# Optimization experiments

Hardware: AMD Instinct MI355X
Metric: run time of the kernel (lower is better)

## Reference

```python
import jax, jax.numpy as jnp
import numpy as np

EPS_MSG = 1e-7   # GENConv message eps
EPS_SM = 1e-16   # scatter_softmax denom eps
EPS_BN = 1e-5    # BatchNorm1d eps


def genconv(x, src, dst, t, W1, W2, gamma, beta):
    """One GENConv (aggr='softmax', learn_t, edge_attr=None, bias=False)."""
    n = x.shape[0]
    # message: relu(x_j) + eps over edges  [E, d]
    msg = jax.nn.relu(x[src]) + EPS_MSG
    # softmax over edges sharing a destination, per feature, temperature t
    logits = msg * t
    m = jax.ops.segment_max(logits, dst, num_segments=n)
    m = jnp.where(jnp.isfinite(m), m, 0.0)          # empty segments -> 0
    w = jnp.exp(logits - m[dst])
    denom = jax.ops.segment_sum(w, dst, num_segments=n) + EPS_SM
    aggr = jax.ops.segment_sum(w * msg, dst, num_segments=n) / denom
    # update: MLP(aggr + x); MLP = Lin(d,2d) -> BN -> ReLU -> Lin(2d,d)
    h = aggr + x
    h1 = h @ W1
    mean = jnp.mean(h1, axis=0)
    var = jnp.var(h1, axis=0)
    h1 = (h1 - mean) * jax.lax.rsqrt(var + EPS_BN) * gamma + beta
    h1 = jax.nn.relu(h1)
    return h1 @ W2


def setup_inputs() -> dict:
    key = jax.random.key(0)
    ks = jax.random.split(key, 4)
    N, E, D = 100000, 800000, 128
    x = jax.random.normal(ks[0], (N, D), dtype=jnp.float32)
    edge_index = jax.random.randint(ks[1], (2, E), 0, N, dtype=jnp.int64)
    t_all = jnp.ones((4,), dtype=jnp.float32)  # learn_t init 1.0
    W1_all = jax.random.normal(ks[2], (4, D, 2 * D), dtype=jnp.float32) * (1.0 / np.sqrt(D))
    W2_all = jax.random.normal(ks[3], (4, 2 * D, D), dtype=jnp.float32) * (1.0 / np.sqrt(2 * D))
    gamma_all = jnp.ones((4, 2 * D), dtype=jnp.float32)
    beta_all = jnp.zeros((4, 2 * D), dtype=jnp.float32)
    return {"x": x, "edge_index": edge_index, "t_all": t_all,
            "W1_all": W1_all, "W2_all": W2_all,
            "gamma_all": gamma_all, "beta_all": beta_all}


def reference(x, edge_index, t_all, W1_all, W2_all, gamma_all, beta_all):
    src, dst = edge_index[0], edge_index[1]
    n_aggr = 2
    h = x
    for i in range(n_aggr):
        h = genconv(h, src, dst, t_all[i], W1_all[i], W2_all[i], gamma_all[i], beta_all[i])
        h = jax.nn.relu(h)
        # dropout: identity (inference)
    mu = genconv(h, src, dst, t_all[2], W1_all[2], W2_all[2], gamma_all[2], beta_all[2])
    logstd = genconv(h, src, dst, t_all[3], W1_all[3], W2_all[3], gamma_all[3], beta_all[3])
    return (mu, logstd)
```

## Files before the change

### kernel.cpp

```cpp
#include <hip/hip_runtime.h>
#include <math.h>

#define D 128
#define H 256
#define NSLOT 64

typedef short s16x8 __attribute__((ext_vector_type(8)));
typedef float f32x4 __attribute__((ext_vector_type(4)));
typedef unsigned int u32x2 __attribute__((ext_vector_type(2)));
typedef unsigned short u16;
typedef unsigned int u32;

__device__ __forceinline__ u16 f2b(float f) {
    union { float f; unsigned u; } c;
    c.f = f;
    unsigned u = c.u + 0x7FFFu + ((c.u >> 16) & 1u);
    return (u16)(u >> 16);
}
__device__ __forceinline__ float b2f(u16 h) {
    union { unsigned u; float f; } c;
    c.u = ((unsigned)h) << 16;
    return c.f;
}
__device__ __forceinline__ float blo(u32 p) {
    union { unsigned u; float f; } c;
    c.u = p << 16;
    return c.f;
}
__device__ __forceinline__ float bhi(u32 p) {
    union { unsigned u; float f; } c;
    c.u = p & 0xFFFF0000u;
    return c.f;
}


__global__ __launch_bounds__(256) void k_count(const int* __restrict__ dstA,
                                               int* __restrict__ deg, int E) {
    int e = blockIdx.x * 256 + threadIdx.x;
    if (e < E) atomicAdd(&deg[dstA[e]], 1);
}

__global__ __launch_bounds__(1024) void k_scan1(const int* __restrict__ deg,
                                                int* __restrict__ rowptr,
                                                int* __restrict__ bsum, int N) {
    __shared__ int tmp[1024];
    int t = threadIdx.x;
    int i = blockIdx.x * 1024 + t;
    int v = (i < N) ? deg[i] : 0;
    tmp[t] = v;
    __syncthreads();
    #pragma unroll
    for (int off = 1; off < 1024; off <<= 1) {
        int u = (t >= off) ? tmp[t - off] : 0;
        __syncthreads();
        tmp[t] += u;
        __syncthreads();
    }
    if (i < N) rowptr[i] = tmp[t] - v;
    if (t == 1023) bsum[blockIdx.x] = tmp[1023];
}

__global__ __launch_bounds__(1024) void k_scan2(int* __restrict__ bsum, int B) {
    __shared__ int sums[1024];
    int t = threadIdx.x;
    int chunk = (B + 1023) >> 10;
    int beg = t * chunk;
    int end = beg + chunk;
    if (end > B) end = B;
    int s = 0;
    for (int i = beg; i < end; ++i) s += bsum[i];
    sums[t] = s;
    __syncthreads();
    #pragma unroll
    for (int off = 1; off < 1024; off <<= 1) {
        int v = (t >= off) ? sums[t - off] : 0;
        __syncthreads();
        sums[t] += v;
        __syncthreads();
    }
    int run = (t == 0) ? 0 : sums[t - 1];
    for (int i = beg; i < end; ++i) {
        int v = bsum[i];
        bsum[i] = run;
        run += v;
    }
}

__global__ __launch_bounds__(1024) void k_scan3(int* __restrict__ rowptr,
                                                const int* __restrict__ bsum,
                                                int* __restrict__ deg,
                                                int N, int E) {
    int i = blockIdx.x * 1024 + threadIdx.x;
    if (i < N) {
        rowptr[i] += bsum[blockIdx.x];
        deg[i] = 0;
    } else if (i == N) {
        rowptr[N] = E;
    }
}

__global__ __launch_bounds__(256) void k_scatter(const int* __restrict__ srcA,
                                                 const int* __restrict__ dstA,
                                                 const int* __restrict__ rowptr,
                                                 int* __restrict__ cnt,
                                                 int* __restrict__ srcs, int E) {
    int e = blockIdx.x * 256 + threadIdx.x;
    if (e < E) {
        int d = dstA[e];
        int p = rowptr[d] + atomicAdd(&cnt[d], 1);
        srcs[p] = srcA[e];
    }
}


__global__ __launch_bounds__(256) void k_cvtprep(const float* __restrict__ x,
                                                 u16* __restrict__ xb,
                                                 const float* __restrict__ W1_all,
                                                 const float* __restrict__ W2_all,
                                                 u16* __restrict__ WT1,
                                                 u16* __restrict__ WT2,
                                                 int* __restrict__ deg,
                                                 int n4, int N) {
    int id = blockIdx.x * 256 + threadIdx.x;
    if (id < N) deg[id] = 0;
    if (id < n4) {
        float4 v = ((const float4*)x)[id];
        xb[id * 4 + 0] = f2b(v.x);
        xb[id * 4 + 1] = f2b(v.y);
        xb[id * 4 + 2] = f2b(v.z);
        xb[id * 4 + 3] = f2b(v.w);
    } else {
        int p = id - n4;
        if (p < 131072) {
            int l = p >> 15, rem = p & 32767, n = rem >> 7, k = rem & 127;
            WT1[p] = f2b(W1_all[l * 32768 + k * 256 + n]);
        } else if (p < 262144) {
            int p2 = p - 131072;
            int l = p2 >> 15, rem = p2 & 32767, n = rem >> 8, k = rem & 255;
            WT2[p2] = f2b(W2_all[l * 32768 + k * 128 + n]);
        }
    }
}


__global__ __launch_bounds__(256) void k_edge(const u16* __restrict__ hin,
                                              const int* __restrict__ rowptr,
                                              const int* __restrict__ srcs,
                                              const float* __restrict__ tptr,
                                              u16* __restrict__ g,
                                              float* __restrict__ psum,
                                              float* __restrict__ pss, int N) {
    if (blockIdx.x < NSLOT) {
        psum[blockIdx.x * 256 + threadIdx.x] = 0.f;
        pss[blockIdx.x * 256 + threadIdx.x] = 0.f;
    }
    int u = blockIdx.x * 4 + (threadIdx.x >> 6);
    if (u >= N) return;
    u = __builtin_amdgcn_readfirstlane(u);
    int lane = threadIdx.x & 63;
    const u32* hin32 = (const u32*)hin;
    float t = *tptr;
    int beg = rowptr[u], end = rowptr[u + 1];
    int cnt = end - beg;

    u32 pu = hin32[(size_t)u * 64 + lane];

    float s0 = 0.f, s1 = 0.f, sn0 = 0.f, sn1 = 0.f;

    for (int b = 0; b < cnt; b += 64) {
        int nb = cnt - b;
        if (nb > 64) nb = 64;
        int sv = (b + lane < cnt) ? srcs[beg + b + lane] : 0;
        for (int ib = 0; ib < nb; ib += 16) {
            int m = nb - ib;
            if (m > 16) m = 16;
            u32 pr[16];
            #pragma unroll
            for (int j = 0; j < 16; ++j) {
                if (j < m) {
                    int vi = __builtin_amdgcn_readlane(sv, ib + j);
                    pr[j] = hin32[(size_t)vi * 64 + lane];
                }
            }
            #pragma unroll
            for (int j = 0; j < 16; ++j) {
                if (j < m) {
                    u32 p = pr[j];
                    float v0 = fmaxf(blo(p), 0.f) + 1e-7f;
                    float v1 = fmaxf(bhi(p), 0.f) + 1e-7f;
                    float w0 = __expf(v0 * t), w1 = __expf(v1 * t);
                    s0 += w0; s1 += w1;
                    sn0 = fmaf(w0, v0, sn0);
                    sn1 = fmaf(w1, v1, sn1);
                }
            }
        }
    }

    bool has = (cnt > 0);
    bool good = (s0 >= 1e-8f) && (s0 <= 1e26f) && (s1 >= 1e-8f) && (s1 <= 1e26f)
                && (sn0 - sn0 == 0.0f) && (sn1 - sn1 == 0.0f);
    if (__any(has && !good)) {
        float m0 = -3.0e38f, m1 = -3.0e38f;
        s0 = s1 = sn0 = sn1 = 0.f;
        for (int e = beg; e < end; ++e) {
            int v = srcs[e];
            u32 p = hin32[(size_t)v * 64 + lane];
            float v0 = fmaxf(blo(p), 0.f) + 1e-7f;
            float v1 = fmaxf(bhi(p), 0.f) + 1e-7f;
            float l0 = v0 * t, l1 = v1 * t;
            float nm0 = fmaxf(m0, l0), nm1 = fmaxf(m1, l1);
            float a0 = __expf(m0 - nm0), a1 = __expf(m1 - nm1);
            float w0 = __expf(l0 - nm0), w1 = __expf(l1 - nm1);
            s0 = s0 * a0 + w0;           s1 = s1 * a1 + w1;
            sn0 = sn0 * a0 + w0 * v0;    sn1 = sn1 * a1 + w1 * v1;
            m0 = nm0; m1 = nm1;
        }
    }

    float aggr0 = sn0 / (s0 + 1e-16f);
    float aggr1 = sn1 / (s1 + 1e-16f);
    float o0 = aggr0 + blo(pu);
    float o1 = aggr1 + bhi(pu);
    ((u32*)g)[(size_t)u * 64 + lane] = (u32)f2b(o0) | ((u32)f2b(o1) << 16);
}


__global__ __launch_bounds__(256) void k_mm1(const u16* __restrict__ A,
                                             const u16* __restrict__ WT,
                                             u16* __restrict__ C,
                                             float* __restrict__ psum,
                                             float* __restrict__ pss, int M) {
    __shared__ u16 As[128][72];
    __shared__ u16 Bs[128][72];
    __shared__ float csumA[128], cssA[128], csumB[128], cssB[128];
    int row0 = blockIdx.x * 128, n0 = blockIdx.y * 128;
    int tid = threadIdx.x;
    int lane = tid & 63, w = tid >> 6;
    int r0w = (w & 1) * 64, c0w = (w >> 1) * 64;
    int q = lane >> 4, ml = lane & 15;

    f32x4 acc[4][4];
    #pragma unroll
    for (int i = 0; i < 4; ++i)
        #pragma unroll
        for (int j = 0; j < 4; ++j) acc[i][j] = f32x4{0.f, 0.f, 0.f, 0.f};

    for (int kk = 0; kk < 128; kk += 64) {
        #pragma unroll
        for (int i = 0; i < 4; ++i) {
            int r = i * 32 + (tid >> 3);
            int c8 = (tid & 7) * 8;
            s16x8 va = s16x8{0, 0, 0, 0, 0, 0, 0, 0};
            if (row0 + r < M)
                va = *reinterpret_cast<const s16x8*>(&A[(size_t)(row0 + r) * 128 + kk + c8]);
            *reinterpret_cast<s16x8*>(&As[r][c8]) = va;
            s16x8 vb = *reinterpret_cast<const s16x8*>(&WT[(size_t)(n0 + r) * 128 + kk + c8]);
            *reinterpret_cast<s16x8*>(&Bs[r][c8]) = vb;
        }
        __syncthreads();
        #pragma unroll
        for (int ks = 0; ks < 64; ks += 32) {
            s16x8 af[4], bfr[4];
            #pragma unroll
            for (int rt = 0; rt < 4; ++rt)
                af[rt] = *reinterpret_cast<const s16x8*>(&As[r0w + rt * 16 + ml][ks + q * 8]);
            #pragma unroll
            for (int ct = 0; ct < 4; ++ct)
                bfr[ct] = *reinterpret_cast<const s16x8*>(&Bs[c0w + ct * 16 + ml][ks + q * 8]);
            #pragma unroll
            for (int rt = 0; rt < 4; ++rt)
                #pragma unroll
                for (int ct = 0; ct < 4; ++ct)
                    acc[rt][ct] = __builtin_amdgcn_mfma_f32_16x16x32_bf16(
                        bfr[ct], af[rt], acc[rt][ct], 0, 0, 0);
        }
        __syncthreads();
    }

    #pragma unroll
    for (int rt = 0; rt < 4; ++rt) {
        int row = row0 + r0w + rt * 16 + ml;
        if (row < M) {
            #pragma unroll
            for (int ct = 0; ct < 4; ++ct) {
                f32x4 a = acc[rt][ct];
                u32x2 p;
                p.x = (u32)f2b(a[0]) | ((u32)f2b(a[1]) << 16);
                p.y = (u32)f2b(a[2]) | ((u32)f2b(a[3]) << 16);
                int col = n0 + c0w + ct * 16 + q * 4;
                *reinterpret_cast<u32x2*>(&C[(size_t)row * H + col]) = p;
            }
        }
    }

    float sp[16], ssp[16];
    #pragma unroll
    for (int ct = 0; ct < 4; ++ct)
        #pragma unroll
        for (int r = 0; r < 4; ++r) {
            float s = 0.f, ss = 0.f;
            #pragma unroll
            for (int rt = 0; rt < 4; ++rt) {
                float v = acc[rt][ct][r];
                s += v;
                ss += v * v;
            }
            sp[ct * 4 + r] = s;
            ssp[ct * 4 + r] = ss;
        }
    #pragma unroll
    for (int msk = 1; msk < 16; msk <<= 1) {
        #pragma unroll
        for (int i = 0; i < 16; ++i) {
            sp[i] += __shfl_xor(sp[i], msk);
            ssp[i] += __shfl_xor(ssp[i], msk);
        }
    }
    if (ml == 0) {
        float* cs = (w & 1) ? csumB : csumA;
        float* cq = (w & 1) ? cssB : cssA;
        #pragma unroll
        for (int ct = 0; ct < 4; ++ct)
            #pragma unroll
            for (int r = 0; r < 4; ++r) {
                int col = c0w + ct * 16 + q * 4 + r;
                cs[col] = sp[ct * 4 + r];
                cq[col] = ssp[ct * 4 + r];
            }
    }
    __syncthreads();
    if (tid < 128) {
        int slot = blockIdx.x & (NSLOT - 1);
        atomicAdd(&psum[(size_t)slot * 256 + n0 + tid], csumA[tid] + csumB[tid]);
        atomicAdd(&pss[(size_t)slot * 256 + n0 + tid], cssA[tid] + cssB[tid]);
    }
}


__global__ __launch_bounds__(256) void k_mm2(const u16* __restrict__ H1,
                                             const float* __restrict__ psum,
                                             const float* __restrict__ pss,
                                             const float* __restrict__ gamma,
                                             const float* __restrict__ beta,
                                             const u16* __restrict__ WT,
                                             float* __restrict__ outf,
                                             u16* __restrict__ outb, int M) {
    __shared__ u16 As[128][72];
    __shared__ u16 Bs[128][72];
    __shared__ float sc_s[H], sh_s[H];
    int row0 = blockIdx.x * 128;
    int tid = threadIdx.x;
    int lane = tid & 63, w = tid >> 6;
    int r0w = (w & 1) * 64, c0w = (w >> 1) * 64;
    int q = lane >> 4, ml = lane & 15;

    {
        float s = 0.f, ss = 0.f;
        #pragma unroll 8
        for (int b = 0; b < NSLOT; ++b) {
            s += psum[b * 256 + tid];
            ss += pss[b * 256 + tid];
        }
        float inv = 1.0f / (float)M;
        float mean = s * inv;
        float var = ss * inv - mean * mean;
        if (var < 0.f) var = 0.f;
        float rstd = rsqrtf(var + 1e-5f);
        float sc = rstd * gamma[tid];
        sc_s[tid] = sc;
        sh_s[tid] = beta[tid] - mean * sc;
    }
    __syncthreads();

    f32x4 acc[4][4];
    #pragma unroll
    for (int i = 0; i < 4; ++i)
        #pragma unroll
        for (int j = 0; j < 4; ++j) acc[i][j] = f32x4{0.f, 0.f, 0.f, 0.f};

    for (int kk = 0; kk < 256; kk += 64) {
        #pragma unroll
        for (int i = 0; i < 4; ++i) {
            int r = i * 32 + (tid >> 3);
            int c8 = (tid & 7) * 8;
            s16x8 o = s16x8{0, 0, 0, 0, 0, 0, 0, 0};
            if (row0 + r < M) {
                s16x8 v = *reinterpret_cast<const s16x8*>(&H1[(size_t)(row0 + r) * H + kk + c8]);
                #pragma unroll
                for (int j = 0; j < 8; ++j) {
                    float f = b2f((u16)v[j]) * sc_s[kk + c8 + j] + sh_s[kk + c8 + j];
                    o[j] = (short)f2b(fmaxf(f, 0.f));
                }
            }
            *reinterpret_cast<s16x8*>(&As[r][c8]) = o;
            s16x8 vb = *reinterpret_cast<const s16x8*>(&WT[(size_t)r * H + kk + c8]);
            *reinterpret_cast<s16x8*>(&Bs[r][c8]) = vb;
        }
        __syncthreads();
        #pragma unroll
        for (int ks = 0; ks < 64; ks += 32) {
            s16x8 af[4], bfr[4];
            #pragma unroll
            for (int rt = 0; rt < 4; ++rt)
                af[rt] = *reinterpret_cast<const s16x8*>(&As[r0w + rt * 16 + ml][ks + q * 8]);
            #pragma unroll
            for (int ct = 0; ct < 4; ++ct)
                bfr[ct] = *reinterpret_cast<const s16x8*>(&Bs[c0w + ct * 16 + ml][ks + q * 8]);
            #pragma unroll
            for (int rt = 0; rt < 4; ++rt)
                #pragma unroll
                for (int ct = 0; ct < 4; ++ct)
                    acc[rt][ct] = __builtin_amdgcn_mfma_f32_16x16x32_bf16(
                        bfr[ct], af[rt], acc[rt][ct], 0, 0, 0);
        }
        __syncthreads();
    }

    #pragma unroll
    for (int rt = 0; rt < 4; ++rt) {
        int row = row0 + r0w + rt * 16 + ml;
        if (row < M) {
            #pragma unroll
            for (int ct = 0; ct < 4; ++ct) {
                f32x4 a = acc[rt][ct];
                int col = c0w + ct * 16 + q * 4;
                if (outb) {
                    u32x2 p;
                    p.x = (u32)f2b(fmaxf(a[0], 0.f)) | ((u32)f2b(fmaxf(a[1], 0.f)) << 16);
                    p.y = (u32)f2b(fmaxf(a[2], 0.f)) | ((u32)f2b(fmaxf(a[3], 0.f)) << 16);
                    *reinterpret_cast<u32x2*>(&outb[(size_t)row * D + col]) = p;
                } else {
                    *reinterpret_cast<f32x4*>(&outf[(size_t)row * D + col]) = a;
                }
            }
        }
    }
}


extern "C" void kernel_launch(void* const* d_in, const int* in_sizes, int n_in,
                              void* d_out, int out_size, void* d_ws, size_t ws_size,
                              hipStream_t stream) {
    const float* x         = (const float*)d_in[0];
    const int*   ei        = (const int*)d_in[1];
    const float* t_all     = (const float*)d_in[2];
    const float* W1_all    = (const float*)d_in[3];
    const float* W2_all    = (const float*)d_in[4];
    const float* gamma_all = (const float*)d_in[5];
    const float* beta_all  = (const float*)d_in[6];

    int N = in_sizes[0] / D;
    int E = in_sizes[1] / 2;
    float* out = (float*)d_out;

    char* ws = (char*)d_ws;
    size_t off = 0;
    auto alloc = [&](size_t bytes) -> void* {
        void* p = ws + off;
        off += (bytes + 255) & ~(size_t)255;
        return p;
    };
    int B = (N + 1023) >> 10;
    int* rowptr = (int*)alloc((size_t)(N + 1) * 4);
    int* deg    = (int*)alloc((size_t)N * 4);
    int* srcs   = (int*)alloc((size_t)E * 4);
    int* bsum   = (int*)alloc((size_t)(B + 1) * 4);
    u16* xb     = (u16*)alloc((size_t)N * D * 2);
    u16* a0     = (u16*)alloc((size_t)N * D * 2);
    u16* a1     = (u16*)alloc((size_t)N * D * 2);
    u16* g      = (u16*)alloc((size_t)N * D * 2);
    u16* h1     = (u16*)alloc((size_t)N * H * 2);
    u16* WT1    = (u16*)alloc((size_t)4 * H * D * 2);
    u16* WT2    = (u16*)alloc((size_t)4 * D * H * 2);
    float* psum = (float*)alloc((size_t)NSLOT * 256 * 4);
    float* pss  = (float*)alloc((size_t)NSLOT * 256 * 4);
    (void)ws_size; (void)n_in; (void)out_size;

    const int* srcA = ei;
    const int* dstA = ei + E;

    int n4 = N * D / 4;
    k_cvtprep<<<(n4 + 262144 + 255) / 256, 256, 0, stream>>>(
        x, xb, W1_all, W2_all, WT1, WT2, deg, n4, N);

    k_count<<<(E + 255) / 256, 256, 0, stream>>>(dstA, deg, E);
    k_scan1<<<B, 1024, 0, stream>>>(deg, rowptr, bsum, N);
    k_scan2<<<1, 1024, 0, stream>>>(bsum, B);
    k_scan3<<<(N + 1 + 1023) / 1024, 1024, 0, stream>>>(rowptr, bsum, deg, N, E);
    k_scatter<<<(E + 255) / 256, 256, 0, stream>>>(srcA, dstA, rowptr, deg, srcs, E);

    float* out0 = out;
    float* out1 = out + (size_t)N * D;

    int gx = (N + 127) / 128;
    for (int layer = 0; layer < 4; ++layer) {
        const u16* hin = (layer == 0) ? xb : (layer == 1 ? a0 : a1);
        k_edge<<<(N + 3) / 4, 256, 0, stream>>>(hin, rowptr, srcs, t_all + layer,
                                                g, psum, pss, N);

        k_mm1<<<dim3(gx, 2), 256, 0, stream>>>(g, WT1 + (size_t)layer * H * D, h1,
                                               psum, pss, N);

        float* outf = nullptr;
        u16*   outb = nullptr;
        if (layer == 0)      outb = a0;
        else if (layer == 1) outb = a1;
        else if (layer == 2) outf = out0;
        else                 outf = out1;

        k_mm2<<<dim3(gx, 1), 256, 0, stream>>>(h1, psum, pss,
                                               gamma_all + (size_t)layer * H,
                                               beta_all + (size_t)layer * H,
                                               WT2 + (size_t)layer * D * H,
                                               outf, outb, N);
    }
}
```

Before: 797.6 us.

## Load MFMA operands directly from global memory, dropping LDS staging in GEMMs

Both GEMM kernels (mm1 and mm2) no longer stage A and W tiles in shared memory with __syncthreads. Each lane now loads its MFMA fragments straight from global memory, with a bounds-checked path for the tail block in mm1 and clamped row pointers in mm2. This removes the LDS round trip and the barriers and should raise occupancy. In exchange, each wave loads data that other waves in the block also load, so the kernels rely more on L1/L2 bandwidth, and mm2 repeats its BN affine transform per wave.

```diff
diff --git a/kernel.cpp b/kernel.cpp
--- a/kernel.cpp
+++ b/kernel.cpp
@@ -231,8 +231,6 @@
                                              u16* __restrict__ C,
                                              float* __restrict__ psum,
                                              float* __restrict__ pss, int M) {
-    __shared__ u16 As[128][72];
-    __shared__ u16 Bs[128][72];
     __shared__ float csumA[128], cssA[128], csumB[128], cssB[128];
     int row0 = blockIdx.x * 128, n0 = blockIdx.y * 128;
     int tid = threadIdx.x;
@@ -246,28 +244,19 @@
         #pragma unroll
         for (int j = 0; j < 4; ++j) acc[i][j] = f32x4{0.f, 0.f, 0.f, 0.f};
 
-    for (int kk = 0; kk < 128; kk += 64) {
-        #pragma unroll
-        for (int i = 0; i < 4; ++i) {
-            int r = i * 32 + (tid >> 3);
-            int c8 = (tid & 7) * 8;
-            s16x8 va = s16x8{0, 0, 0, 0, 0, 0, 0, 0};
-            if (row0 + r < M)
-                va = *reinterpret_cast<const s16x8*>(&A[(size_t)(row0 + r) * 128 + kk + c8]);
-            *reinterpret_cast<s16x8*>(&As[r][c8]) = va;
-            s16x8 vb = *reinterpret_cast<const s16x8*>(&WT[(size_t)(n0 + r) * 128 + kk + c8]);
-            *reinterpret_cast<s16x8*>(&Bs[r][c8]) = vb;
-        }
-        __syncthreads();
-        #pragma unroll
-        for (int ks = 0; ks < 64; ks += 32) {
+    const u16* Ab = A + (size_t)(row0 + r0w + ml) * D + q * 8;
+    const u16* Bb = WT + (size_t)(n0 + c0w + ml) * D + q * 8;
+
+    if (row0 + 128 <= M) {
+        #pragma unroll 2
+        for (int ks = 0; ks < 128; ks += 32) {
             s16x8 af[4], bfr[4];
             #pragma unroll
             for (int rt = 0; rt < 4; ++rt)
-                af[rt] = *reinterpret_cast<const s16x8*>(&As[r0w + rt * 16 + ml][ks + q * 8]);
+                af[rt] = *reinterpret_cast<const s16x8*>(&Ab[(size_t)rt * 16 * D + ks]);
             #pragma unroll
             for (int ct = 0; ct < 4; ++ct)
-                bfr[ct] = *reinterpret_cast<const s16x8*>(&Bs[c0w + ct * 16 + ml][ks + q * 8]);
+                bfr[ct] = *reinterpret_cast<const s16x8*>(&Bb[(size_t)ct * 16 * D + ks]);
             #pragma unroll
             for (int rt = 0; rt < 4; ++rt)
                 #pragma unroll
@@ -275,7 +264,27 @@
                     acc[rt][ct] = __builtin_amdgcn_mfma_f32_16x16x32_bf16(
                         bfr[ct], af[rt], acc[rt][ct], 0, 0, 0);
         }
-        __syncthreads();
+    } else {
+        #pragma unroll 2
+        for (int ks = 0; ks < 128; ks += 32) {
+            s16x8 af[4], bfr[4];
+            #pragma unroll
+            for (int rt = 0; rt < 4; ++rt) {
+                int row = row0 + r0w + rt * 16 + ml;
+                af[rt] = (row < M)
+                    ? *reinterpret_cast<const s16x8*>(&Ab[(size_t)rt * 16 * D + ks])
+                    : s16x8{0, 0, 0, 0, 0, 0, 0, 0};
+            }
+            #pragma unroll
+            for (int ct = 0; ct < 4; ++ct)
+                bfr[ct] = *reinterpret_cast<const s16x8*>(&Bb[(size_t)ct * 16 * D + ks]);
+            #pragma unroll
+            for (int rt = 0; rt < 4; ++rt)
+                #pragma unroll
+                for (int ct = 0; ct < 4; ++ct)
+                    acc[rt][ct] = __builtin_amdgcn_mfma_f32_16x16x32_bf16(
+                        bfr[ct], af[rt], acc[rt][ct], 0, 0, 0);
+        }
     }
 
     #pragma unroll
@@ -346,8 +355,6 @@
                                              const u16* __restrict__ WT,
                                              float* __restrict__ outf,
                                              u16* __restrict__ outb, int M) {
-    __shared__ u16 As[128][72];
-    __shared__ u16 Bs[128][72];
     __shared__ float sc_s[H], sh_s[H];
     int row0 = blockIdx.x * 128;
     int tid = threadIdx.x;
@@ -379,42 +386,39 @@
         #pragma unroll
         for (int j = 0; j < 4; ++j) acc[i][j] = f32x4{0.f, 0.f, 0.f, 0.f};
 
-    for (int kk = 0; kk < 256; kk += 64) {
-        #pragma unroll
-        for (int i = 0; i < 4; ++i) {
-            int r = i * 32 + (tid >> 3);
-            int c8 = (tid & 7) * 8;
-            s16x8 o = s16x8{0, 0, 0, 0, 0, 0, 0, 0};
-            if (row0 + r < M) {
-                s16x8 v = *reinterpret_cast<const s16x8*>(&H1[(size_t)(row0 + r) * H + kk + c8]);
-                #pragma unroll
-                for (int j = 0; j < 8; ++j) {
-                    float f = b2f((u16)v[j]) * sc_s[kk + c8 + j] + sh_s[kk + c8 + j];
-                    o[j] = (short)f2b(fmaxf(f, 0.f));
-                }
-            }
-            *reinterpret_cast<s16x8*>(&As[r][c8]) = o;
-            s16x8 vb = *reinterpret_cast<const s16x8*>(&WT[(size_t)r * H + kk + c8]);
-            *reinterpret_cast<s16x8*>(&Bs[r][c8]) = vb;
-        }
-        __syncthreads();
-        #pragma unroll
-        for (int ks = 0; ks < 64; ks += 32) {
-            s16x8 af[4], bfr[4];
-            #pragma unroll
-            for (int rt = 0; rt < 4; ++rt)
-                af[rt] = *reinterpret_cast<const s16x8*>(&As[r0w + rt * 16 + ml][ks + q * 8]);
+    const u16* Ab[4];
+    #pragma unroll
+    for (int rt = 0; rt < 4; ++rt) {
+        int row = row0 + r0w + rt * 16 + ml;
+        if (row >= M) row = M - 1;
+        Ab[rt] = H1 + (size_t)row * H + q * 8;
+    }
+    const u16* Bb = WT + (size_t)(c0w + ml) * H + q * 8;
+
+    #pragma unroll 2
+    for (int ks = 0; ks < 256; ks += 32) {
+        s16x8 af[4], bfr[4];
+        #pragma unroll
+        for (int rt = 0; rt < 4; ++rt) {
+            s16x8 v = *reinterpret_cast<const s16x8*>(&Ab[rt][ks]);
+            s16x8 o;
+            int k0 = ks + q * 8;
+            #pragma unroll
+            for (int j = 0; j < 8; ++j) {
+                float f = b2f((u16)v[j]) * sc_s[k0 + j] + sh_s[k0 + j];
+                o[j] = (short)f2b(fmaxf(f, 0.f));
+            }
+            af[rt] = o;
+        }
+        #pragma unroll
+        for (int ct = 0; ct < 4; ++ct)
+            bfr[ct] = *reinterpret_cast<const s16x8*>(&Bb[(size_t)ct * 16 * H + ks]);
+        #pragma unroll
+        for (int rt = 0; rt < 4; ++rt)
             #pragma unroll
             for (int ct = 0; ct < 4; ++ct)
-                bfr[ct] = *reinterpret_cast<const s16x8*>(&Bs[c0w + ct * 16 + ml][ks + q * 8]);
-            #pragma unroll
-            for (int rt = 0; rt < 4; ++rt)
-                #pragma unroll
-                for (int ct = 0; ct < 4; ++ct)
-                    acc[rt][ct] = __builtin_amdgcn_mfma_f32_16x16x32_bf16(
-                        bfr[ct], af[rt], acc[rt][ct], 0, 0, 0);
-        }
-        __syncthreads();
+                acc[rt][ct] = __builtin_amdgcn_mfma_f32_16x16x32_bf16(
+                    bfr[ct], af[rt], acc[rt][ct], 0, 0, 0);
     }
 
     #pragma unroll
```

After: 844.3 us. 1.06x slower.
